# Kernel optimization log

Measured on AMD Instinct MI355X. Metric: run time of the kernel, lower is better.

Reference implementation:

```python
import jax, jax.numpy as jnp
import numpy as np

HIDDEN = 4096
HEAD_DIM = 128
N_HEADS = 32
N_KV_HEADS = 8
ROPE_THETA = 10000.0


def setup_inputs() -> dict:
    key = jax.random.key(0)
    k1, k2, k3 = jax.random.split(key, 3)
    qkv_dim = (N_HEADS + 2 * N_KV_HEADS) * HEAD_DIM  # 6144
    x = jax.random.normal(k1, (2, 2048, HIDDEN), dtype=jnp.float32)
    w_qkv = jax.random.normal(k2, (HIDDEN, qkv_dim), dtype=jnp.float32) * (HIDDEN ** -0.5)
    w_out = jax.random.normal(k3, (N_HEADS * HEAD_DIM, HIDDEN), dtype=jnp.float32) * ((N_HEADS * HEAD_DIM) ** -0.5)
    return {"x": x, "w_qkv": w_qkv, "w_out": w_out}


def _apply_rope(t):
    # t: [B, S, H, D], rotate over full head dim (half-split convention)
    B, S, H, D = t.shape
    half = D // 2
    inv_freq = 1.0 / (ROPE_THETA ** (jnp.arange(0, half, dtype=jnp.float32) / half))
    freqs = jnp.arange(S, dtype=jnp.float32)[:, None] * inv_freq[None, :]  # [S, D/2]
    cos = jnp.cos(freqs)[None, :, None, :].astype(t.dtype)
    sin = jnp.sin(freqs)[None, :, None, :].astype(t.dtype)
    t1, t2 = t[..., :half], t[..., half:]
    return jnp.concatenate([t1 * cos - t2 * sin, t1 * sin + t2 * cos], axis=-1)


def reference(x, w_qkv, w_out):
    B, S, _ = x.shape
    qkv = x @ w_qkv  # [B, S, (H + 2*Hkv) * D]
    qkv = qkv.reshape(B, S, N_HEADS + 2 * N_KV_HEADS, HEAD_DIM)
    q = qkv[:, :, :N_HEADS]                                 # [B,S,H,D]
    k = qkv[:, :, N_HEADS:N_HEADS + N_KV_HEADS]             # [B,S,Hkv,D]
    v = qkv[:, :, N_HEADS + N_KV_HEADS:]                    # [B,S,Hkv,D]
    q = _apply_rope(q)
    k = _apply_rope(k)
    # GQA: expand KV heads to match query heads
    group = N_HEADS // N_KV_HEADS
    k = jnp.repeat(k, group, axis=2)  # [B,S,H,D]
    v = jnp.repeat(v, group, axis=2)
    q = q.transpose(0, 2, 1, 3)  # [B,H,S,D]
    k = k.transpose(0, 2, 1, 3)
    v = v.transpose(0, 2, 1, 3)
    scale = HEAD_DIM ** -0.5
    scores = jnp.einsum('bhqd,bhkd->bhqk', q, k) * scale  # [B,H,S,S]
    probs = jax.nn.softmax(scores, axis=-1)
    out = jnp.einsum('bhqk,bhkd->bhqd', probs, v)  # [B,H,S,D]
    out = out.transpose(0, 2, 1, 3).reshape(B, S, N_HEADS * HEAD_DIM)
    return out @ w_out  # [B,S,hidden]
```

## Files before the change

kernel.cpp:

```cpp
#include <hip/hip_runtime.h>

typedef unsigned short u16;
typedef float f32x4 __attribute__((ext_vector_type(4)));
typedef __bf16 bf16x8 __attribute__((ext_vector_type(8)));

__device__ __forceinline__ u16 f2bf(float f) {
  union { float f; unsigned int u; } x; x.f = f;
  unsigned int u = x.u;
  u += 0x7fffu + ((u >> 16) & 1u);
  return (u16)(u >> 16);
}
__device__ __forceinline__ float bf2f(u16 h) {
  union { unsigned int u; float f; } x; x.u = ((unsigned int)h) << 16;
  return x.f;
}
#if __has_builtin(__builtin_amdgcn_exp2f)
__device__ __forceinline__ float exp2_hw(float x) { return __builtin_amdgcn_exp2f(x); }
#else
__device__ __forceinline__ float exp2_hw(float x) { return exp2f(x); }
#endif
__device__ __forceinline__ void load_lds16(const void* g, void* l) {
  __builtin_amdgcn_global_load_lds(
      (const __attribute__((address_space(1))) unsigned int*)g,
      (__attribute__((address_space(3))) unsigned int*)l, 16, 0, 0);
}
__device__ __forceinline__ f32x4 mfma16(bf16x8 a, bf16x8 b, f32x4 c) {
  return __builtin_amdgcn_mfma_f32_16x16x32_bf16(a, b, c, 0, 0, 0);
}
__device__ __forceinline__ void bar() { __builtin_amdgcn_s_barrier(); }
template <int Nw> __device__ __forceinline__ void waitvm() {
  if constexpr (Nw == 8)      asm volatile("s_waitcnt vmcnt(8)" ::: "memory");
  else if constexpr (Nw == 6) asm volatile("s_waitcnt vmcnt(6)" ::: "memory");
  else if constexpr (Nw == 4) asm volatile("s_waitcnt vmcnt(4)" ::: "memory");
  else                        asm volatile("s_waitcnt vmcnt(0)" ::: "memory");
}
__device__ __forceinline__ void phase_open() {
  asm volatile("" ::: "memory");
  __builtin_amdgcn_s_barrier();
  asm volatile("s_waitcnt lgkmcnt(0)" ::: "memory");
  __builtin_amdgcn_sched_barrier(0);
  __builtin_amdgcn_s_setprio(1);
}
__device__ __forceinline__ void phase_close() {
  __builtin_amdgcn_s_setprio(0);
  asm volatile("" ::: "memory");
  __builtin_amdgcn_s_barrier();
  asm volatile("" ::: "memory");
}
template <int NV> __device__ __forceinline__ void phase_close_vm() {
  __builtin_amdgcn_s_setprio(0);
  asm volatile("" ::: "memory");
  waitvm<NV>();
  __builtin_amdgcn_s_barrier();
  asm volatile("" ::: "memory");
}

__global__ void convert4(const float* __restrict__ in, u16* __restrict__ out) {
  int i = blockIdx.x * blockDim.x + threadIdx.x;
  float4 v = reinterpret_cast<const float4*>(in)[i];
  ushort4 o;
  o.x = f2bf(v.x); o.y = f2bf(v.y); o.z = f2bf(v.z); o.w = f2bf(v.w);
  reinterpret_cast<ushort4*>(out)[i] = o;
}

__global__ void transpose_f32_bf16(const float* __restrict__ in, u16* __restrict__ out,
                                   int R, int Cd) {
  __shared__ float tile[32][33];
  int c0 = blockIdx.x * 32, r0 = blockIdx.y * 32;
  int tx = threadIdx.x, ty = threadIdx.y;
#pragma unroll
  for (int i = 0; i < 4; ++i)
    tile[ty + 8 * i][tx] = in[(size_t)(r0 + ty + 8 * i) * Cd + c0 + tx];
  __syncthreads();
#pragma unroll
  for (int i = 0; i < 4; ++i)
    out[(size_t)(c0 + ty + 8 * i) * R + r0 + tx] = f2bf(tile[tx][ty + 8 * i]);
}

__global__ void rope_table(float2* __restrict__ tab) {
  int i = blockIdx.x * blockDim.x + threadIdx.x;
  int s = i >> 6, d2 = i & 63;
  float inv = powf(10000.f, -(float)d2 * (1.f / 64.f));
  float fr = (float)s * inv;
  tab[i] = make_float2(cosf(fr), sinf(fr));
}

__global__ void rope_apply(u16* __restrict__ qkv, const float2* __restrict__ tab) {
  int i = blockIdx.x * blockDim.x + threadIdx.x;
  int d2 = i & 63;
  int head = (i >> 6) % 40;
  int row = i / 2560;
  size_t base = (size_t)row * 6144 + head * 128 + d2;
  float t1 = bf2f(qkv[base]), t2 = bf2f(qkv[base + 64]);
  float2 cs = tab[(row & 2047) * 64 + d2];
  float o1 = t1 * cs.x - t2 * cs.y;
  float o2 = t1 * cs.y + t2 * cs.x;
  float sc = (head < 32) ? 0.12751731654059898f : 1.f;
  qkv[base]      = f2bf(o1 * sc);
  qkv[base + 64] = f2bf(o2 * sc);
}

__global__ void build_vT(const u16* __restrict__ qkv, u16* __restrict__ vT) {
  __shared__ u16 tile[32][33];
  int st = blockIdx.x, dt = blockIdx.y, bh = blockIdx.z;
  int b = bh >> 3, hkv = bh & 7;
  int tx = threadIdx.x, ty = threadIdx.y;
  int s0 = st * 32, d0 = dt * 32;
#pragma unroll
  for (int i = 0; i < 4; ++i)
    tile[ty + 8 * i][tx] =
        qkv[(size_t)(b * 2048 + s0 + ty + 8 * i) * 6144 + 5120 + hkv * 128 + d0 + tx];
  __syncthreads();
  int s = s0 + tx;
  int sl = s & 63;
  int sp = (s & ~63) | (sl & 0x23) | ((sl & 0x0C) << 1) | ((sl & 0x10) >> 2);
#pragma unroll
  for (int i = 0; i < 4; ++i)
    vT[((size_t)bh * 128 + d0 + ty + 8 * i) * 2048 + sp] = tile[tx][ty + 8 * i];
}

template <int OUT_BF16>
__global__ __launch_bounds__(512, 2) void gemm256x256(const u16* __restrict__ A,
                                                      const u16* __restrict__ BT,
                                                      void* __restrict__ Cv,
                                                      int M, int N, int K) {
  __shared__ u16 As[2][256][64];
  __shared__ u16 Bs[2][256][64];
  const int tid = threadIdx.x, lane = tid & 63, wave = tid >> 6;
  const int lr = lane & 15, lg = lane >> 4, l7 = lane & 7;
  const int wm = wave >> 2, wn = wave & 3;
  const int nbx = N / 256;
  int bid = blockIdx.x;
  const int cpx = (int)gridDim.x >> 3;
  bid = (bid & 7) * cpx + (bid >> 3);
  const int bm = (bid / nbx) * 256, bn = (bid % nbx) * 256;
  const int NT = K / 64;
  const int ch0 = (lg ^ l7) << 3, ch1 = ((4 | lg) ^ l7) << 3;

  auto stageA = [&](int t) {
    int c2 = t & 1, k0 = t * 64;
#pragma unroll
    for (int o = 0; o < 4; ++o) {
      int cid = o * 512 + tid;
      int row = cid >> 3;
      int sc2 = (cid & 7) ^ (row & 7);
      load_lds16(A + (size_t)(bm + row) * K + k0 + sc2 * 8,
                 (u16*)&As[c2][0][0] + (o * 512 + wave * 64) * 8);
    }
  };
  auto stageB = [&](int t) {
    int c2 = t & 1, k0 = t * 64;
#pragma unroll
    for (int o = 0; o < 4; ++o) {
      int cid = o * 512 + tid;
      int row = cid >> 3;
      int sc2 = (cid & 7) ^ (row & 7);
      load_lds16(BT + (size_t)(bn + row) * K + k0 + sc2 * 8,
                 (u16*)&Bs[c2][0][0] + (o * 512 + wave * 64) * 8);
    }
  };

  bf16x8 a0[4][2], a1[4][2], b01[2][2], b23[2][2];
  f32x4 acc[8][4] = {};

  stageA(0); stageB(0); stageA(1); stageB(1);
  waitvm<8>();
  bar();
#pragma unroll
  for (int mi = 0; mi < 4; ++mi) {
    a0[mi][0] = *(const bf16x8*)&As[0][wm * 128 + mi * 16 + lr][ch0];
    a0[mi][1] = *(const bf16x8*)&As[0][wm * 128 + mi * 16 + lr][ch1];
  }
#pragma unroll
  for (int j = 0; j < 2; ++j) {
    b01[j][0] = *(const bf16x8*)&Bs[0][wn * 64 + j * 16 + lr][ch0];
    b01[j][1] = *(const bf16x8*)&Bs[0][wn * 64 + j * 16 + lr][ch1];
  }

  for (int t = 0; t < NT; ++t) {
    const int c = t & 1, cn = c ^ 1;
    const bool pf = (t + 2) < NT;
#pragma unroll
    for (int j = 0; j < 2; ++j) {
      b23[j][0] = *(const bf16x8*)&Bs[c][wn * 64 + (j + 2) * 16 + lr][ch0];
      b23[j][1] = *(const bf16x8*)&Bs[c][wn * 64 + (j + 2) * 16 + lr][ch1];
    }
    phase_open();
#pragma unroll
    for (int mi = 0; mi < 4; ++mi)
#pragma unroll
      for (int j = 0; j < 2; ++j) {
        acc[mi][j] = mfma16(a0[mi][0], b01[j][0], acc[mi][j]);
        acc[mi][j] = mfma16(a0[mi][1], b01[j][1], acc[mi][j]);
      }
    phase_close();
#pragma unroll
    for (int mi = 0; mi < 4; ++mi) {
      a1[mi][0] = *(const bf16x8*)&As[c][wm * 128 + 64 + mi * 16 + lr][ch0];
      a1[mi][1] = *(const bf16x8*)&As[c][wm * 128 + 64 + mi * 16 + lr][ch1];
    }
    if (pf) stageB(t + 2);
    phase_open();
#pragma unroll
    for (int mi = 0; mi < 4; ++mi)
#pragma unroll
      for (int j = 0; j < 2; ++j) {
        acc[mi][j + 2] = mfma16(a0[mi][0], b23[j][0], acc[mi][j + 2]);
        acc[mi][j + 2] = mfma16(a0[mi][1], b23[j][1], acc[mi][j + 2]);
      }
    if (pf) phase_close_vm<4>(); else phase_close_vm<0>();
#pragma unroll
    for (int mi = 0; mi < 4; ++mi) {
      a0[mi][0] = *(const bf16x8*)&As[cn][wm * 128 + mi * 16 + lr][ch0];
      a0[mi][1] = *(const bf16x8*)&As[cn][wm * 128 + mi * 16 + lr][ch1];
    }
    if (pf) stageA(t + 2);
    phase_open();
#pragma unroll
    for (int mi = 0; mi < 4; ++mi)
#pragma unroll
      for (int j = 0; j < 2; ++j) {
        acc[mi + 4][j] = mfma16(a1[mi][0], b01[j][0], acc[mi + 4][j]);
        acc[mi + 4][j] = mfma16(a1[mi][1], b01[j][1], acc[mi + 4][j]);
      }
    phase_close();
#pragma unroll
    for (int j = 0; j < 2; ++j) {
      b01[j][0] = *(const bf16x8*)&Bs[cn][wn * 64 + j * 16 + lr][ch0];
      b01[j][1] = *(const bf16x8*)&Bs[cn][wn * 64 + j * 16 + lr][ch1];
    }
    phase_open();
#pragma unroll
    for (int mi = 0; mi < 4; ++mi)
#pragma unroll
      for (int j = 0; j < 2; ++j) {
        acc[mi + 4][j + 2] = mfma16(a1[mi][0], b23[j][0], acc[mi + 4][j + 2]);
        acc[mi + 4][j + 2] = mfma16(a1[mi][1], b23[j][1], acc[mi + 4][j + 2]);
      }
    phase_close();
  }
#pragma unroll
  for (int mi = 0; mi < 8; ++mi) {
    int row = bm + wm * 128 + mi * 16 + lg * 4;
#pragma unroll
    for (int j = 0; j < 4; ++j) {
      int col = bn + wn * 64 + j * 16 + lr;
#pragma unroll
      for (int r = 0; r < 4; ++r) {
        if constexpr (OUT_BF16)
          ((u16*)Cv)[(size_t)(row + r) * N + col] = f2bf(acc[mi][j][r]);
        else
          ((float*)Cv)[(size_t)(row + r) * N + col] = acc[mi][j][r];
      }
    }
  }
}

#define G1_TILE(T, C, CUR, NXT)                                               \
  {                                                                           \
    const bool pf = ((T) + 2) < NT;                                           \
    _Pragma("unroll")                                                         \
    for (int j = 0; j < 2; ++j) {                                             \
      b23[j][0] = *(const bf16x8*)&Bs[C][wn * 64 + (j + 2) * 16 + lr][ch0];   \
      b23[j][1] = *(const bf16x8*)&Bs[C][wn * 64 + (j + 2) * 16 + lr][ch1];   \
    }                                                                         \
    if (pf) stageA((T) + 2);                                                  \
    phase_open();                                                             \
    _Pragma("unroll")                                                         \
    for (int mi = 0; mi < 4; ++mi)                                            \
      _Pragma("unroll")                                                       \
      for (int j = 0; j < 2; ++j) {                                           \
        acc[mi][j] = mfma16(CUR[mi][0], b01[j][0], acc[mi][j]);               \
        acc[mi][j] = mfma16(CUR[mi][1], b01[j][1], acc[mi][j]);               \
      }                                                                       \
    if (pf) phase_close_vm<4>(); else phase_close_vm<0>();                    \
    _Pragma("unroll")                                                         \
    for (int mi = 0; mi < 4; ++mi) {                                          \
      NXT[mi][0] = *(const bf16x8*)&As[(C) ^ 1][wm * 64 + mi * 16 + lr][ch0]; \
      NXT[mi][1] = *(const bf16x8*)&As[(C) ^ 1][wm * 64 + mi * 16 + lr][ch1]; \
    }                                                                         \
    _Pragma("unroll")                                                         \
    for (int j = 0; j < 2; ++j) {                                             \
      b01[j][0] = *(const bf16x8*)&Bs[(C) ^ 1][wn * 64 + j * 16 + lr][ch0];   \
      b01[j][1] = *(const bf16x8*)&Bs[(C) ^ 1][wn * 64 + j * 16 + lr][ch1];   \
    }                                                                         \
    if (pf) stageB((T) + 2);                                                  \
    phase_open();                                                             \
    _Pragma("unroll")                                                         \
    for (int mi = 0; mi < 4; ++mi)                                            \
      _Pragma("unroll")                                                       \
      for (int j = 0; j < 2; ++j) {                                           \
        acc[mi][j + 2] = mfma16(CUR[mi][0], b23[j][0], acc[mi][j + 2]);       \
        acc[mi][j + 2] = mfma16(CUR[mi][1], b23[j][1], acc[mi][j + 2]);       \
      }                                                                       \
    phase_close();                                                            \
  }

template <int OUT_BF16>
__global__ __launch_bounds__(512, 2) void gemm256x128(const u16* __restrict__ A,
                                                      const u16* __restrict__ BT,
                                                      void* __restrict__ Cv,
                                                      int M, int N, int K) {
  __shared__ u16 As[2][256][64];
  __shared__ u16 Bs[2][128][64];
  const int tid = threadIdx.x, lane = tid & 63, wave = tid >> 6;
  const int lr = lane & 15, lg = lane >> 4, l7 = lane & 7;
  const int wm = wave >> 1, wn = wave & 1;
  const int nbx = N / 128;
  int bid = blockIdx.x;
  const int cpx = (int)gridDim.x >> 3;
  bid = (bid & 7) * cpx + (bid >> 3);
  const int bm = (bid / nbx) * 256, bn = (bid % nbx) * 128;
  const int NT = K / 64;
  const int ch0 = (lg ^ l7) << 3, ch1 = ((4 | lg) ^ l7) << 3;

  auto stageA = [&](int t) {
    int c2 = t & 1, k0 = t * 64;
#pragma unroll
    for (int o = 0; o < 4; ++o) {
      int cid = o * 512 + tid;
      int row = cid >> 3;
      int sc2 = (cid & 7) ^ (row & 7);
      load_lds16(A + (size_t)(bm + row) * K + k0 + sc2 * 8,
                 (u16*)&As[c2][0][0] + (o * 512 + wave * 64) * 8);
    }
  };
  auto stageB = [&](int t) {
    int c2 = t & 1, k0 = t * 64;
#pragma unroll
    for (int o = 0; o < 2; ++o) {
      int cid = o * 512 + tid;
      int row = cid >> 3;
      int sc2 = (cid & 7) ^ (row & 7);
      load_lds16(BT + (size_t)(bn + row) * K + k0 + sc2 * 8,
                 (u16*)&Bs[c2][0][0] + (o * 512 + wave * 64) * 8);
    }
  };

  bf16x8 Aa[4][2], Ab[4][2], b01[2][2], b23[2][2];
  f32x4 acc[4][4] = {};

  stageA(0); stageB(0); stageA(1); stageB(1);
  waitvm<6>();
  bar();
#pragma unroll
  for (int mi = 0; mi < 4; ++mi) {
    Aa[mi][0] = *(const bf16x8*)&As[0][wm * 64 + mi * 16 + lr][ch0];
    Aa[mi][1] = *(const bf16x8*)&As[0][wm * 64 + mi * 16 + lr][ch1];
  }
#pragma unroll
  for (int j = 0; j < 2; ++j) {
    b01[j][0] = *(const bf16x8*)&Bs[0][wn * 64 + j * 16 + lr][ch0];
    b01[j][1] = *(const bf16x8*)&Bs[0][wn * 64 + j * 16 + lr][ch1];
  }

  for (int tt = 0; tt < NT; tt += 2) {
    G1_TILE(tt, 0, Aa, Ab);
    G1_TILE(tt + 1, 1, Ab, Aa);
  }
#pragma unroll
  for (int mi = 0; mi < 4; ++mi) {
    int row = bm + wm * 64 + mi * 16 + lg * 4;
#pragma unroll
    for (int j = 0; j < 4; ++j) {
      int col = bn + wn * 64 + j * 16 + lr;
#pragma unroll
      for (int r = 0; r < 4; ++r) {
        if constexpr (OUT_BF16)
          ((u16*)Cv)[(size_t)(row + r) * N + col] = f2bf(acc[mi][j][r]);
        else
          ((float*)Cv)[(size_t)(row + r) * N + col] = acc[mi][j][r];
      }
    }
  }
}

__global__ __launch_bounds__(256, 3) void attn_fused(const u16* __restrict__ qkv,
                                                     const u16* __restrict__ vT,
                                                     u16* __restrict__ attn_out) {
  __shared__ u16 Ksm[64][128];
  __shared__ u16 Vsm[128][64];
  const int qt = blockIdx.x, h = blockIdx.y, b = blockIdx.z;
  const int hkv = h >> 2;
  const int tid = threadIdx.x, lane = tid & 63, wave = tid >> 6;
  const int lr = lane & 15, lg = lane >> 4;
  const int qrow0 = qt * 128 + wave * 32;

  bf16x8 qf[2][4];
#pragma unroll
  for (int q2 = 0; q2 < 2; ++q2) {
    const u16* qp = qkv + (size_t)(b * 2048 + qrow0 + q2 * 16 + lr) * 6144 + h * 128;
#pragma unroll
    for (int kk = 0; kk < 4; ++kk)
      qf[q2][kk] = *(const bf16x8*)(qp + kk * 32 + lg * 8);
  }
  float l_acc[2] = {0.f, 0.f};
  f32x4 acc_o[2][8] = {};

  for (int kv0 = 0; kv0 < 2048; kv0 += 64) {
#pragma unroll
    for (int c = 0; c < 4; ++c) {
      int cid = c * 256 + tid;
      int base = (c * 256 + wave * 64) * 8;
      int krow = cid >> 4;
      int kcc = (cid & 15) ^ (krow & 7);
      load_lds16(qkv + (size_t)(b * 2048 + kv0 + krow) * 6144 + 4096 + hkv * 128 + kcc * 8,
                 (u16*)Ksm + base);
      int vrow = cid >> 3;
      int vcc = (cid & 7) ^ (vrow & 7);
      load_lds16(vT + ((size_t)(b * 8 + hkv) * 128 + vrow) * 2048 + kv0 + vcc * 8,
                 (u16*)Vsm + base);
    }
    __syncthreads();

    bf16x8 pfr[2][2];
#pragma unroll
    for (int k2 = 0; k2 < 2; ++k2) {
      f32x4 sc[2][2] = {};
#pragma unroll
      for (int ktl = 0; ktl < 2; ++ktl) {
        int krow = (k2 * 2 + ktl) * 16 + lr;
#pragma unroll
        for (int kk = 0; kk < 4; ++kk) {
          bf16x8 kf = *(const bf16x8*)((u16*)Ksm + krow * 128 +
                                       ((((kk << 2) | lg) ^ (krow & 7)) << 3));
          sc[0][ktl] = mfma16(kf, qf[0][kk], sc[0][ktl]);
          sc[1][ktl] = mfma16(kf, qf[1][kk], sc[1][ktl]);
        }
      }
#pragma unroll
      for (int q2 = 0; q2 < 2; ++q2) {
        bf16x8 pk;
#pragma unroll
        for (int ktl = 0; ktl < 2; ++ktl)
#pragma unroll
          for (int r = 0; r < 4; ++r) {
            float e = exp2_hw(sc[q2][ktl][r]);
            l_acc[q2] += e;
            pk[ktl * 4 + r] = (__bf16)e;
          }
        pfr[q2][k2] = pk;
      }
    }
#pragma unroll
    for (int dt = 0; dt < 8; ++dt) {
      int vrow = dt * 16 + lr;
#pragma unroll
      for (int k2 = 0; k2 < 2; ++k2) {
        bf16x8 vf = *(const bf16x8*)((u16*)Vsm + vrow * 64 +
                                     ((((k2 << 2) | lg) ^ (vrow & 7)) << 3));
        acc_o[0][dt] = mfma16(pfr[0][k2], vf, acc_o[0][dt]);
        acc_o[1][dt] = mfma16(pfr[1][k2], vf, acc_o[1][dt]);
      }
    }
    __syncthreads();
  }
#pragma unroll
  for (int q2 = 0; q2 < 2; ++q2) {
    float l = l_acc[q2];
    l += __shfl_xor(l, 16);
    l += __shfl_xor(l, 32);
    float li = 1.f / l;
    float linv[4];
#pragma unroll
    for (int r = 0; r < 4; ++r) linv[r] = __shfl(li, lg * 4 + r);
    u16* op = attn_out + (size_t)(b * 2048 + qrow0 + q2 * 16) * 4096 + h * 128;
#pragma unroll
    for (int dt = 0; dt < 8; ++dt)
#pragma unroll
      for (int r = 0; r < 4; ++r)
        op[(size_t)(lg * 4 + r) * 4096 + dt * 16 + lr] = f2bf(acc_o[q2][dt][r] * linv[r]);
  }
}

extern "C" void kernel_launch(void* const* d_in, const int* in_sizes, int n_in,
                              void* d_out, int out_size, void* d_ws, size_t ws_size,
                              hipStream_t stream) {
  const float* x     = (const float*)d_in[0];
  const float* w_qkv = (const float*)d_in[1];
  const float* w_out = (const float*)d_in[2];
  float* out = (float*)d_out;
  char* ws = (char*)d_ws;

  u16*    xbf = (u16*)(ws);
  u16*    wT  = (u16*)(ws + (size_t)33554432);
  u16*    qkv = (u16*)(ws + (size_t)83886080);
  u16*    vT  = (u16*)(ws + (size_t)134217728);
  float2* tab = (float2*)(ws + (size_t)142606336);

  dim3 tb(32, 8);
  convert4<<<16384, 256, 0, stream>>>(x, xbf);
  transpose_f32_bf16<<<dim3(192, 128), tb, 0, stream>>>(w_qkv, wT, 4096, 6144);
  rope_table<<<512, 256, 0, stream>>>(tab);
  gemm256x128<1><<<768, 512, 0, stream>>>(xbf, wT, qkv, 4096, 6144, 4096);
  rope_apply<<<40960, 256, 0, stream>>>(qkv, tab);
  build_vT<<<dim3(64, 4, 16), tb, 0, stream>>>(qkv, vT);
  attn_fused<<<dim3(16, 32, 2), 256, 0, stream>>>(qkv, vT, xbf);
  transpose_f32_bf16<<<dim3(128, 128), tb, 0, stream>>>(w_out, wT, 4096, 4096);
  gemm256x256<0><<<256, 512, 0, stream>>>(xbf, wT, out, 4096, 4096, 4096);
}
```

Before: 626.5 us.

## Triple-buffer QKV GEMM LDS and restage output GEMM prefetch pipeline

The QKV projection GEMM moves from double-buffered to triple-buffered LDS (3x256x64 A, 3x128x64 B). Each K-tile's fragments are now read at the start of the iteration while tile t+2 is prefetched into the third buffer, which removes the cross-iteration register prefetch. The output GEMM keeps two buffers but splits the B staging into halves and issues the t+2 loads into the current buffer after its fragments are consumed, with one vmcnt wait per iteration. The aim is fewer barriers and stalls and more overlap of global loads with MFMA, at the cost of more LDS per block (which may hurt occupancy with 2 blocks per CU) and less register-level prefetch.

```diff
diff --git a/kernel.cpp b/kernel.cpp
--- a/kernel.cpp
+++ b/kernel.cpp
@@ -120,10 +120,116 @@
 }
 
 template <int OUT_BF16>
-__global__ __launch_bounds__(512, 2) void gemm256x256(const u16* __restrict__ A,
-                                                      const u16* __restrict__ BT,
-                                                      void* __restrict__ Cv,
-                                                      int M, int N, int K) {
+__global__ __launch_bounds__(512, 2) void gemm_g1(const u16* __restrict__ A,
+                                                  const u16* __restrict__ BT,
+                                                  void* __restrict__ Cv,
+                                                  int M, int N, int K) {
+  __shared__ u16 As[3][256][64];
+  __shared__ u16 Bs[3][128][64];
+  const int tid = threadIdx.x, lane = tid & 63, wave = tid >> 6;
+  const int lr = lane & 15, lg = lane >> 4, l7 = lane & 7;
+  const int wm = wave >> 1, wn = wave & 1;
+  const int nbx = N / 128;
+  int bid = blockIdx.x;
+  const int cpx = (int)gridDim.x >> 3;
+  bid = (bid & 7) * cpx + (bid >> 3);
+  const int bm = (bid / nbx) * 256, bn = (bid % nbx) * 128;
+  const int NT = K / 64;
+  const int ch0 = (lg ^ l7) << 3, ch1 = ((4 | lg) ^ l7) << 3;
+
+  auto stageA = [&](int t, int rg) {
+    int k0 = t * 64;
+#pragma unroll
+    for (int o = 0; o < 4; ++o) {
+      int cid = o * 512 + tid;
+      int row = cid >> 3;
+      int sc2 = (cid & 7) ^ (row & 7);
+      load_lds16(A + (size_t)(bm + row) * K + k0 + sc2 * 8,
+                 (u16*)&As[rg][0][0] + (o * 512 + wave * 64) * 8);
+    }
+  };
+  auto stageB = [&](int t, int rg) {
+    int k0 = t * 64;
+#pragma unroll
+    for (int o = 0; o < 2; ++o) {
+      int cid = o * 512 + tid;
+      int row = cid >> 3;
+      int sc2 = (cid & 7) ^ (row & 7);
+      load_lds16(BT + (size_t)(bn + row) * K + k0 + sc2 * 8,
+                 (u16*)&Bs[rg][0][0] + (o * 512 + wave * 64) * 8);
+    }
+  };
+
+  bf16x8 af[4][2], b01[2][2], b23[2][2];
+  f32x4 acc[4][4] = {};
+
+  stageB(0, 0); stageA(0, 0); stageB(1, 1); stageA(1, 1);
+  waitvm<6>();
+  bar();
+
+  int c = 0;
+  for (int t = 0; t < NT; ++t) {
+    int cs = c + 2; if (cs >= 3) cs -= 3;
+    const bool pf = (t + 2) < NT;
+#pragma unroll
+    for (int mi = 0; mi < 4; ++mi) {
+      af[mi][0] = *(const bf16x8*)&As[c][wm * 64 + mi * 16 + lr][ch0];
+      af[mi][1] = *(const bf16x8*)&As[c][wm * 64 + mi * 16 + lr][ch1];
+    }
+#pragma unroll
+    for (int j = 0; j < 2; ++j) {
+      b01[j][0] = *(const bf16x8*)&Bs[c][wn * 64 + j * 16 + lr][ch0];
+      b01[j][1] = *(const bf16x8*)&Bs[c][wn * 64 + j * 16 + lr][ch1];
+    }
+    if (pf) stageB(t + 2, cs);
+    phase_open();
+#pragma unroll
+    for (int mi = 0; mi < 4; ++mi)
+#pragma unroll
+      for (int j = 0; j < 2; ++j) {
+        acc[mi][j] = mfma16(af[mi][0], b01[j][0], acc[mi][j]);
+        acc[mi][j] = mfma16(af[mi][1], b01[j][1], acc[mi][j]);
+      }
+    phase_close();
+#pragma unroll
+    for (int j = 0; j < 2; ++j) {
+      b23[j][0] = *(const bf16x8*)&Bs[c][wn * 64 + (j + 2) * 16 + lr][ch0];
+      b23[j][1] = *(const bf16x8*)&Bs[c][wn * 64 + (j + 2) * 16 + lr][ch1];
+    }
+    if (pf) stageA(t + 2, cs);
+    phase_open();
+#pragma unroll
+    for (int mi = 0; mi < 4; ++mi)
+#pragma unroll
+      for (int j = 0; j < 2; ++j) {
+        acc[mi][j + 2] = mfma16(af[mi][0], b23[j][0], acc[mi][j + 2]);
+        acc[mi][j + 2] = mfma16(af[mi][1], b23[j][1], acc[mi][j + 2]);
+      }
+    if (pf) phase_close_vm<6>(); else phase_close_vm<0>();
+    c = c + 1; if (c >= 3) c -= 3;
+  }
+#pragma unroll
+  for (int mi = 0; mi < 4; ++mi) {
+    int row = bm + wm * 64 + mi * 16 + lg * 4;
+#pragma unroll
+    for (int j = 0; j < 4; ++j) {
+      int col = bn + wn * 64 + j * 16 + lr;
+#pragma unroll
+      for (int r = 0; r < 4; ++r) {
+        if constexpr (OUT_BF16)
+          ((u16*)Cv)[(size_t)(row + r) * N + col] = f2bf(acc[mi][j][r]);
+        else
+          ((float*)Cv)[(size_t)(row + r) * N + col] = acc[mi][j][r];
+      }
+    }
+  }
+}
+
+template <int OUT_BF16>
+__global__ __launch_bounds__(512, 2) void gemm_g2(const u16* __restrict__ A,
+                                                  const u16* __restrict__ BT,
+                                                  void* __restrict__ Cv,
+                                                  int M, int N, int K) {
   __shared__ u16 As[2][256][64];
   __shared__ u16 Bs[2][256][64];
   const int tid = threadIdx.x, lane = tid & 63, wave = tid >> 6;
@@ -137,49 +243,60 @@
   const int NT = K / 64;
   const int ch0 = (lg ^ l7) << 3, ch1 = ((4 | lg) ^ l7) << 3;
 
-  auto stageA = [&](int t) {
-    int c2 = t & 1, k0 = t * 64;
+  auto stageA = [&](int t, int rg) {
+    int k0 = t * 64;
 #pragma unroll
     for (int o = 0; o < 4; ++o) {
       int cid = o * 512 + tid;
       int row = cid >> 3;
       int sc2 = (cid & 7) ^ (row & 7);
       load_lds16(A + (size_t)(bm + row) * K + k0 + sc2 * 8,
-                 (u16*)&As[c2][0][0] + (o * 512 + wave * 64) * 8);
+                 (u16*)&As[rg][0][0] + (o * 512 + wave * 64) * 8);
     }
   };
-  auto stageB = [&](int t) {
-    int c2 = t & 1, k0 = t * 64;
-#pragma unroll
-    for (int o = 0; o < 4; ++o) {
-      int cid = o * 512 + tid;
+  auto stageBh = [&](int t, int rg, int h) {
+    int k0 = t * 64;
+#pragma unroll
+    for (int o = 0; o < 2; ++o) {
+      int oo = h * 2 + o;
+      int cid = oo * 512 + tid;
       int row = cid >> 3;
       int sc2 = (cid & 7) ^ (row & 7);
       load_lds16(BT + (size_t)(bn + row) * K + k0 + sc2 * 8,
-                 (u16*)&Bs[c2][0][0] + (o * 512 + wave * 64) * 8);
+                 (u16*)&Bs[rg][0][0] + (oo * 512 + wave * 64) * 8);
     }
   };
 
   bf16x8 a0[4][2], a1[4][2], b01[2][2], b23[2][2];
   f32x4 acc[8][4] = {};
 
-  stageA(0); stageB(0); stageA(1); stageB(1);
+  stageA(0, 0); stageBh(0, 0, 0); stageBh(0, 0, 1); stageA(1, 1);
+  stageBh(1, 1, 0); stageBh(1, 1, 1);
   waitvm<8>();
   bar();
-#pragma unroll
-  for (int mi = 0; mi < 4; ++mi) {
-    a0[mi][0] = *(const bf16x8*)&As[0][wm * 128 + mi * 16 + lr][ch0];
-    a0[mi][1] = *(const bf16x8*)&As[0][wm * 128 + mi * 16 + lr][ch1];
-  }
-#pragma unroll
-  for (int j = 0; j < 2; ++j) {
-    b01[j][0] = *(const bf16x8*)&Bs[0][wn * 64 + j * 16 + lr][ch0];
-    b01[j][1] = *(const bf16x8*)&Bs[0][wn * 64 + j * 16 + lr][ch1];
-  }
 
   for (int t = 0; t < NT; ++t) {
-    const int c = t & 1, cn = c ^ 1;
+    const int c = t & 1;
     const bool pf = (t + 2) < NT;
+#pragma unroll
+    for (int mi = 0; mi < 4; ++mi) {
+      a0[mi][0] = *(const bf16x8*)&As[c][wm * 128 + mi * 16 + lr][ch0];
+      a0[mi][1] = *(const bf16x8*)&As[c][wm * 128 + mi * 16 + lr][ch1];
+    }
+#pragma unroll
+    for (int j = 0; j < 2; ++j) {
+      b01[j][0] = *(const bf16x8*)&Bs[c][wn * 64 + j * 16 + lr][ch0];
+      b01[j][1] = *(const bf16x8*)&Bs[c][wn * 64 + j * 16 + lr][ch1];
+    }
+    phase_open();
+#pragma unroll
+    for (int mi = 0; mi < 4; ++mi)
+#pragma unroll
+      for (int j = 0; j < 2; ++j) {
+        acc[mi][j] = mfma16(a0[mi][0], b01[j][0], acc[mi][j]);
+        acc[mi][j] = mfma16(a0[mi][1], b01[j][1], acc[mi][j]);
+      }
+    phase_close();
 #pragma unroll
     for (int j = 0; j < 2; ++j) {
       b23[j][0] = *(const bf16x8*)&Bs[c][wn * 64 + (j + 2) * 16 + lr][ch0];
@@ -190,8 +307,8 @@
     for (int mi = 0; mi < 4; ++mi)
 #pragma unroll
       for (int j = 0; j < 2; ++j) {
-        acc[mi][j] = mfma16(a0[mi][0], b01[j][0], acc[mi][j]);
-        acc[mi][j] = mfma16(a0[mi][1], b01[j][1], acc[mi][j]);
+        acc[mi][j + 2] = mfma16(a0[mi][0], b23[j][0], acc[mi][j + 2]);
+        acc[mi][j + 2] = mfma16(a0[mi][1], b23[j][1], acc[mi][j + 2]);
       }
     phase_close();
 #pragma unroll
@@ -199,22 +316,7 @@
       a1[mi][0] = *(const bf16x8*)&As[c][wm * 128 + 64 + mi * 16 + lr][ch0];
       a1[mi][1] = *(const bf16x8*)&As[c][wm * 128 + 64 + mi * 16 + lr][ch1];
     }
-    if (pf) stageB(t + 2);
-    phase_open();
-#pragma unroll
-    for (int mi = 0; mi < 4; ++mi)
-#pragma unroll
-      for (int j = 0; j < 2; ++j) {
-        acc[mi][j + 2] = mfma16(a0[mi][0], b23[j][0], acc[mi][j + 2]);
-        acc[mi][j + 2] = mfma16(a0[mi][1], b23[j][1], acc[mi][j + 2]);
-      }
-    if (pf) phase_close_vm<4>(); else phase_close_vm<0>();
-#pragma unroll
-    for (int mi = 0; mi < 4; ++mi) {
-      a0[mi][0] = *(const bf16x8*)&As[cn][wm * 128 + mi * 16 + lr][ch0];
-      a0[mi][1] = *(const bf16x8*)&As[cn][wm * 128 + mi * 16 + lr][ch1];
-    }
-    if (pf) stageA(t + 2);
+    if (pf) stageBh(t + 2, c, 0);
     phase_open();
 #pragma unroll
     for (int mi = 0; mi < 4; ++mi)
@@ -224,11 +326,7 @@
         acc[mi + 4][j] = mfma16(a1[mi][1], b01[j][1], acc[mi + 4][j]);
       }
     phase_close();
-#pragma unroll
-    for (int j = 0; j < 2; ++j) {
-      b01[j][0] = *(const bf16x8*)&Bs[cn][wn * 64 + j * 16 + lr][ch0];
-      b01[j][1] = *(const bf16x8*)&Bs[cn][wn * 64 + j * 16 + lr][ch1];
-    }
+    if (pf) { stageBh(t + 2, c, 1); stageA(t + 2, c); }
     phase_open();
 #pragma unroll
     for (int mi = 0; mi < 4; ++mi)
@@ -237,130 +335,11 @@
         acc[mi + 4][j + 2] = mfma16(a1[mi][0], b23[j][0], acc[mi + 4][j + 2]);
         acc[mi + 4][j + 2] = mfma16(a1[mi][1], b23[j][1], acc[mi + 4][j + 2]);
       }
-    phase_close();
+    if (pf) phase_close_vm<8>(); else phase_close_vm<0>();
   }
 #pragma unroll
   for (int mi = 0; mi < 8; ++mi) {
     int row = bm + wm * 128 + mi * 16 + lg * 4;
-#pragma unroll
-    for (int j = 0; j < 4; ++j) {
-      int col = bn + wn * 64 + j * 16 + lr;
-#pragma unroll
-      for (int r = 0; r < 4; ++r) {
-        if constexpr (OUT_BF16)
-          ((u16*)Cv)[(size_t)(row + r) * N + col] = f2bf(acc[mi][j][r]);
-        else
-          ((float*)Cv)[(size_t)(row + r) * N + col] = acc[mi][j][r];
-      }
-    }
-  }
-}
-
-#define G1_TILE(T, C, CUR, NXT)                                               \
-  {                                                                           \
-    const bool pf = ((T) + 2) < NT;                                           \
-    _Pragma("unroll")                                                         \
-    for (int j = 0; j < 2; ++j) {                                             \
-      b23[j][0] = *(const bf16x8*)&Bs[C][wn * 64 + (j + 2) * 16 + lr][ch0];   \
-      b23[j][1] = *(const bf16x8*)&Bs[C][wn * 64 + (j + 2) * 16 + lr][ch1];   \
-    }                                                                         \
-    if (pf) stageA((T) + 2);                                                  \
-    phase_open();                                                             \
-    _Pragma("unroll")                                                         \
-    for (int mi = 0; mi < 4; ++mi)                                            \
-      _Pragma("unroll")                                                       \
-      for (int j = 0; j < 2; ++j) {                                           \
-        acc[mi][j] = mfma16(CUR[mi][0], b01[j][0], acc[mi][j]);               \
-        acc[mi][j] = mfma16(CUR[mi][1], b01[j][1], acc[mi][j]);               \
-      }                                                                       \
-    if (pf) phase_close_vm<4>(); else phase_close_vm<0>();                    \
-    _Pragma("unroll")                                                         \
-    for (int mi = 0; mi < 4; ++mi) {                                          \
-      NXT[mi][0] = *(const bf16x8*)&As[(C) ^ 1][wm * 64 + mi * 16 + lr][ch0]; \
-      NXT[mi][1] = *(const bf16x8*)&As[(C) ^ 1][wm * 64 + mi * 16 + lr][ch1]; \
-    }                                                                         \
-    _Pragma("unroll")                                                         \
-    for (int j = 0; j < 2; ++j) {                                             \
-      b01[j][0] = *(const bf16x8*)&Bs[(C) ^ 1][wn * 64 + j * 16 + lr][ch0];   \
-      b01[j][1] = *(const bf16x8*)&Bs[(C) ^ 1][wn * 64 + j * 16 + lr][ch1];   \
-    }                                                                         \
-    if (pf) stageB((T) + 2);                                                  \
-    phase_open();                                                             \
-    _Pragma("unroll")                                                         \
-    for (int mi = 0; mi < 4; ++mi)                                            \
-      _Pragma("unroll")                                                       \
-      for (int j = 0; j < 2; ++j) {                                           \
-        acc[mi][j + 2] = mfma16(CUR[mi][0], b23[j][0], acc[mi][j + 2]);       \
-        acc[mi][j + 2] = mfma16(CUR[mi][1], b23[j][1], acc[mi][j + 2]);       \
-      }                                                                       \
-    phase_close();                                                            \
-  }
-
-template <int OUT_BF16>
-__global__ __launch_bounds__(512, 2) void gemm256x128(const u16* __restrict__ A,
-                                                      const u16* __restrict__ BT,
-                                                      void* __restrict__ Cv,
-                                                      int M, int N, int K) {
-  __shared__ u16 As[2][256][64];
-  __shared__ u16 Bs[2][128][64];
-  const int tid = threadIdx.x, lane = tid & 63, wave = tid >> 6;
-  const int lr = lane & 15, lg = lane >> 4, l7 = lane & 7;
-  const int wm = wave >> 1, wn = wave & 1;
-  const int nbx = N / 128;
-  int bid = blockIdx.x;
-  const int cpx = (int)gridDim.x >> 3;
-  bid = (bid & 7) * cpx + (bid >> 3);
-  const int bm = (bid / nbx) * 256, bn = (bid % nbx) * 128;
-  const int NT = K / 64;
-  const int ch0 = (lg ^ l7) << 3, ch1 = ((4 | lg) ^ l7) << 3;
-
-  auto stageA = [&](int t) {
-    int c2 = t & 1, k0 = t * 64;
-#pragma unroll
-    for (int o = 0; o < 4; ++o) {
-      int cid = o * 512 + tid;
-      int row = cid >> 3;
-      int sc2 = (cid & 7) ^ (row & 7);
-      load_lds16(A + (size_t)(bm + row) * K + k0 + sc2 * 8,
-                 (u16*)&As[c2][0][0] + (o * 512 + wave * 64) * 8);
-    }
-  };
-  auto stageB = [&](int t) {
-    int c2 = t & 1, k0 = t * 64;
-#pragma unroll
-    for (int o = 0; o < 2; ++o) {
-      int cid = o * 512 + tid;
-      int row = cid >> 3;
-      int sc2 = (cid & 7) ^ (row & 7);
-      load_lds16(BT + (size_t)(bn + row) * K + k0 + sc2 * 8,
-                 (u16*)&Bs[c2][0][0] + (o * 512 + wave * 64) * 8);
-    }
-  };
-
-  bf16x8 Aa[4][2], Ab[4][2], b01[2][2], b23[2][2];
-  f32x4 acc[4][4] = {};
-
-  stageA(0); stageB(0); stageA(1); stageB(1);
-  waitvm<6>();
-  bar();
-#pragma unroll
-  for (int mi = 0; mi < 4; ++mi) {
-    Aa[mi][0] = *(const bf16x8*)&As[0][wm * 64 + mi * 16 + lr][ch0];
-    Aa[mi][1] = *(const bf16x8*)&As[0][wm * 64 + mi * 16 + lr][ch1];
-  }
-#pragma unroll
-  for (int j = 0; j < 2; ++j) {
-    b01[j][0] = *(const bf16x8*)&Bs[0][wn * 64 + j * 16 + lr][ch0];
-    b01[j][1] = *(const bf16x8*)&Bs[0][wn * 64 + j * 16 + lr][ch1];
-  }
-
-  for (int tt = 0; tt < NT; tt += 2) {
-    G1_TILE(tt, 0, Aa, Ab);
-    G1_TILE(tt + 1, 1, Ab, Aa);
-  }
-#pragma unroll
-  for (int mi = 0; mi < 4; ++mi) {
-    int row = bm + wm * 64 + mi * 16 + lg * 4;
 #pragma unroll
     for (int j = 0; j < 4; ++j) {
       int col = bn + wn * 64 + j * 16 + lr;
@@ -492,10 +471,10 @@
   convert4<<<16384, 256, 0, stream>>>(x, xbf);
   transpose_f32_bf16<<<dim3(192, 128), tb, 0, stream>>>(w_qkv, wT, 4096, 6144);
   rope_table<<<512, 256, 0, stream>>>(tab);
-  gemm256x128<1><<<768, 512, 0, stream>>>(xbf, wT, qkv, 4096, 6144, 4096);
+  gemm_g1<1><<<768, 512, 0, stream>>>(xbf, wT, qkv, 4096, 6144, 4096);
   rope_apply<<<40960, 256, 0, stream>>>(qkv, tab);
   build_vT<<<dim3(64, 4, 16), tb, 0, stream>>>(qkv, vT);
   attn_fused<<<dim3(16, 32, 2), 256, 0, stream>>>(qkv, vT, xbf);
   transpose_f32_bf16<<<dim3(128, 128), tb, 0, stream>>>(w_out, wT, 4096, 4096);
-  gemm256x256<0><<<256, 512, 0, stream>>>(xbf, wT, out, 4096, 4096, 4096);
-}
+  gemm_g2<0><<<256, 512, 0, stream>>>(xbf, wT, out, 4096, 4096, 4096);
+}
```

Measured after the change: 591.7 us. 5.6% less time.
